# Optimization experiments

Hardware: AMD Instinct MI355X
Metric: run time of the kernel (lower is better)

## Reference

```python
import jax, jax.numpy as jnp
import numpy as np

B, N, H_IN, H_HID, N_HEAD = 32, 500, 64, 16, 8
N_VALID = 400  # valid (non-padded) nodes per graph; node 0 is the root
NEG_INF = -1e20


def setup_inputs() -> dict:
    key = jax.random.key(0)
    ks = jax.random.split(key, 10)
    x = jax.random.normal(ks[0], (B, N, H_IN), jnp.float32)
    # sparse-ish binary adjacency with self loops
    A = (jax.random.uniform(ks[1], (B, N, N)) < 0.05).astype(jnp.float32)
    A = jnp.maximum(A, jnp.eye(N, dtype=jnp.float32)[None])
    # mask_nonzero: first N_VALID nodes of every graph are valid
    mask_batch = jnp.repeat(jnp.arange(B, dtype=jnp.int32), N_VALID)
    mask_row = jnp.tile(jnp.arange(N_VALID, dtype=jnp.int32), B)
    s = 0.1
    w1 = jax.random.normal(ks[2], (N_HEAD, H_IN, H_HID), jnp.float32) * s
    a_src1 = jax.random.normal(ks[3], (N_HEAD, H_HID), jnp.float32) * s
    a_dst1 = jax.random.normal(ks[4], (N_HEAD, H_HID), jnp.float32) * s
    w2 = jax.random.normal(ks[5], (1, N_HEAD * H_HID, H_IN), jnp.float32) * s
    a_src2 = jax.random.normal(ks[6], (1, H_IN), jnp.float32) * s
    a_dst2 = jax.random.normal(ks[7], (1, H_IN), jnp.float32) * s
    attn_w = jax.random.normal(ks[8], (2 * H_IN,), jnp.float32) * s
    return {"x": x, "A": A, "mask_batch": mask_batch, "mask_row": mask_row,
            "w1": w1, "a_src1": a_src1, "a_dst1": a_dst1,
            "w2": w2, "a_src2": a_src2, "a_dst2": a_dst2, "attn_w": attn_w}


def gat_layer(h_in, A, w, a_src, a_dst):
    # h_in: [B,N,F_in]; w: [H,F_in,F_out]
    h = jnp.einsum('bnf,hfo->bhno', h_in, w)              # [B,H,N,F_out]
    e_src = jnp.einsum('bhno,ho->bhn', h, a_src)          # [B,H,N]
    e_dst = jnp.einsum('bhno,ho->bhn', h, a_dst)
    e = jax.nn.leaky_relu(e_src[..., :, None] + e_dst[..., None, :], 0.2)  # [B,H,N,N]
    e = jnp.where(A[:, None, :, :] > 0, e, NEG_INF)
    attn = jax.nn.softmax(e, axis=-1)
    return jnp.einsum('bhnm,bhmo->bhno', attn, h)         # [B,H,N,F_out]


def reference(x, A, mask_batch, mask_row, w1, a_src1, a_dst1, w2, a_src2, a_dst2, attn_w):
    b, n, _ = x.shape
    # BatchGAT encoder: layer 1 (multi-head, concat + ELU), layer 2 (1 head -> h_in)
    h1 = gat_layer(x, A, w1, a_src1, a_dst1)                       # [B,H,N,h_hid]
    h1 = jax.nn.elu(h1).transpose(0, 2, 1, 3).reshape(b, n, -1)    # [B,N,H*h_hid]
    xc = gat_layer(h1, A, w2, a_src2, a_dst2)[:, 0]                # [B,N,h_in]
    # zero out padded nodes (so their Post_Attn scores are exactly 0)
    valid = jnp.zeros((b, n), x.dtype).at[mask_batch, mask_row].set(1.0)
    xc = xc * valid[:, :, None]
    # Post_Attn: scatter root features to each valid node position
    root = jnp.zeros_like(xc).at[mask_batch, mask_row, :].set(xc[mask_batch, 0, :])
    x_plus = jnp.concatenate([xc, root], axis=-1)                  # [B,N,2*h_in]
    score = x_plus @ attn_w                                        # [B,N]
    score = jnp.where(score == 0, NEG_INF, score)[:, :, None]      # masked_fill
    attn = jax.nn.softmax(score, axis=1)                           # softmax over nodes
    pooled = jnp.einsum('bnf,bn->bf', xc, attn[:, :, 0])           # [B,h_in]
    return pooled, attn
```

## Files before the change

kernel.cpp:

```cpp
#include <hip/hip_runtime.h>

#define NB 32
#define NN 500
#define HIN 64
#define HHID 16
#define NHEAD 8
#define NVALID 400
#define MAXK 128
#define NEG_INF -1e20f

__global__ __launch_bounds__(256) void k_nbr(const float* __restrict__ A,
                                             int* __restrict__ nbr, int* __restrict__ cnt)
{
    int row = blockIdx.x * 4 + (threadIdx.x >> 6);
    int lane = threadIdx.x & 63;
    if (row >= NB * NN) return;
    const float* arow = A + (size_t)row * NN;
    int c = 0;
    for (int it = 0; it < 8; ++it) {
        int m = it * 64 + lane;
        bool v = (m < NN) && (arow[m] > 0.0f);
        unsigned long long bal = __ballot(v);
        if (v) {
            int pos = c + __popcll(bal & ((1ull << lane) - 1ull));
            if (pos < MAXK) nbr[(size_t)row * MAXK + pos] = m;
        }
        c += (int)__popcll(bal);
    }
    if (lane == 0) cnt[row] = c < MAXK ? c : MAXK;
}

__global__ __launch_bounds__(256) void k_proj1(const float* __restrict__ x, const float* __restrict__ w1,
                                               const float* __restrict__ as1, const float* __restrict__ ad1,
                                               float* __restrict__ h1p, float* __restrict__ e1s,
                                               float* __restrict__ e1d)
{
    int b = blockIdx.y, chunk = blockIdx.x;
    int t = threadIdx.x, slot = t >> 7, lane = t & 127;
    int h = lane >> 4, o = lane & 15;
    float wreg[64];
#pragma unroll
    for (int f = 0; f < 64; ++f) wreg[f] = w1[h * 1024 + f * 16 + o];
    float as_r = as1[h * 16 + o], ad_r = ad1[h * 16 + o];
    __shared__ __align__(16) float xs[2][64];
    for (int i = 0; i < 8; ++i) {
        int n = chunk * 16 + i * 2 + slot;
        bool valid = n < NN;
        if (valid && lane < 64) xs[slot][lane] = x[(size_t)(b * NN + n) * HIN + lane];
        __syncthreads();
        if (valid) {
            float acc = 0.f;
#pragma unroll
            for (int f4 = 0; f4 < 16; ++f4) {
                float4 xv = *(const float4*)&xs[slot][f4 * 4];
                acc += xv.x * wreg[f4 * 4] + xv.y * wreg[f4 * 4 + 1]
                     + xv.z * wreg[f4 * 4 + 2] + xv.w * wreg[f4 * 4 + 3];
            }
            h1p[((size_t)(b * NHEAD + h) * NN + n) * HHID + o] = acc;
            float vs = acc * as_r, vd = acc * ad_r;
#pragma unroll
            for (int m = 1; m < 16; m <<= 1) { vs += __shfl_xor(vs, m); vd += __shfl_xor(vd, m); }
            if (o == 0) {
                e1s[(size_t)(b * NHEAD + h) * NN + n] = vs;
                e1d[(size_t)(b * NHEAD + h) * NN + n] = vd;
            }
        }
        __syncthreads();
    }
}

__global__ __launch_bounds__(128) void k_agg1(const int* __restrict__ nbr, const int* __restrict__ cnt,
                                              const float* __restrict__ h1p, const float* __restrict__ e1s,
                                              const float* __restrict__ e1d, float* __restrict__ h1cat)
{
    int row = blockIdx.x;
    int b = row / NN, n = row - b * NN;
    int t = threadIdx.x;
    __shared__ int nb_s[MAXK];
    __shared__ float p_s[NHEAD][MAXK];
    __shared__ float stat[NHEAD][2];
    int K = cnt[row];
    for (int k = t; k < K; k += 128) nb_s[k] = nbr[(size_t)row * MAXK + k];
    __syncthreads();
    for (int idx = t; idx < NHEAD * K; idx += 128) {
        int h = idx / K, k = idx - h * K;
        float e = e1s[(size_t)(b * NHEAD + h) * NN + n]
                + e1d[(size_t)(b * NHEAD + h) * NN + nb_s[k]];
        p_s[h][k] = e > 0.f ? e : 0.2f * e;
    }
    __syncthreads();
    if (t < NHEAD) {
        float mx = -1e30f;
        for (int k = 0; k < K; ++k) mx = fmaxf(mx, p_s[t][k]);
        float sum = 0.f;
        for (int k = 0; k < K; ++k) sum += __expf(p_s[t][k] - mx);
        stat[t][0] = mx; stat[t][1] = 1.f / sum;
    }
    __syncthreads();
    for (int idx = t; idx < NHEAD * K; idx += 128) {
        int h = idx / K, k = idx - h * K;
        p_s[h][k] = __expf(p_s[h][k] - stat[h][0]) * stat[h][1];
    }
    __syncthreads();
    int h = t >> 4, o = t & 15;
    float acc = 0.f;
    const float* hp = h1p + (size_t)(b * NHEAD + h) * NN * HHID + o;
    for (int k = 0; k < K; ++k) acc += p_s[h][k] * hp[(size_t)nb_s[k] * HHID];
    float outv = acc > 0.f ? acc : expm1f(acc);
    h1cat[(size_t)row * (NHEAD * HHID) + t] = outv;
}

__global__ __launch_bounds__(256) void k_proj2(const float* __restrict__ h1cat, const float* __restrict__ w2,
                                               const float* __restrict__ as2, const float* __restrict__ ad2,
                                               float* __restrict__ h2p, float* __restrict__ e2s,
                                               float* __restrict__ e2d)
{
    int b = blockIdx.y, chunk = blockIdx.x;
    int t = threadIdx.x, slot = t >> 7, lane = t & 127;
    int fh = lane >> 6, o = lane & 63;
    float wreg[64];
#pragma unroll
    for (int j = 0; j < 64; ++j) wreg[j] = w2[(fh * 64 + j) * 64 + o];
    float as_r = as2[o], ad_r = ad2[o];
    __shared__ __align__(16) float xs[2][128];
    __shared__ float part[2][128];
    for (int i = 0; i < 8; ++i) {
        int n = chunk * 16 + i * 2 + slot;
        bool valid = n < NN;
        if (valid) xs[slot][lane] = h1cat[(size_t)(b * NN + n) * 128 + lane];
        __syncthreads();
        float acc = 0.f;
        if (valid) {
#pragma unroll
            for (int j4 = 0; j4 < 16; ++j4) {
                float4 xv = *(const float4*)&xs[slot][fh * 64 + j4 * 4];
                acc += xv.x * wreg[j4 * 4] + xv.y * wreg[j4 * 4 + 1]
                     + xv.z * wreg[j4 * 4 + 2] + xv.w * wreg[j4 * 4 + 3];
            }
        }
        part[slot][lane] = acc;
        __syncthreads();
        if (valid && fh == 0) {
            float val = acc + part[slot][64 + o];
            h2p[(size_t)(b * NN + n) * 64 + o] = val;
            float vs = val * as_r, vd = val * ad_r;
#pragma unroll
            for (int m = 1; m < 64; m <<= 1) { vs += __shfl_xor(vs, m); vd += __shfl_xor(vd, m); }
            if (o == 0) { e2s[b * NN + n] = vs; e2d[b * NN + n] = vd; }
        }
        __syncthreads();
    }
}

__global__ __launch_bounds__(64) void k_agg2(const int* __restrict__ nbr, const int* __restrict__ cnt,
                                             const float* __restrict__ h2p, const float* __restrict__ e2s,
                                             const float* __restrict__ e2d, const float* __restrict__ aw,
                                             float* __restrict__ xc, float* __restrict__ sc,
                                             float* __restrict__ root_dot)
{
    int row = blockIdx.x;
    int b = row / NN, n = row - b * NN;
    int t = threadIdx.x;
    if (n >= NVALID) { xc[(size_t)row * 64 + t] = 0.f; return; }
    __shared__ int nb_s[MAXK];
    __shared__ float p_s[MAXK];
    __shared__ float stat[2];
    int K = cnt[row];
    for (int k = t; k < K; k += 64) nb_s[k] = nbr[(size_t)row * MAXK + k];
    __syncthreads();
    float es = e2s[row];
    for (int k = t; k < K; k += 64) {
        float e = es + e2d[b * NN + nb_s[k]];
        p_s[k] = e > 0.f ? e : 0.2f * e;
    }
    __syncthreads();
    if (t == 0) {
        float mx = -1e30f;
        for (int k = 0; k < K; ++k) mx = fmaxf(mx, p_s[k]);
        float sum = 0.f;
        for (int k = 0; k < K; ++k) sum += __expf(p_s[k] - mx);
        stat[0] = mx; stat[1] = 1.f / sum;
    }
    __syncthreads();
    for (int k = t; k < K; k += 64) p_s[k] = __expf(p_s[k] - stat[0]) * stat[1];
    __syncthreads();
    float acc = 0.f;
    for (int k = 0; k < K; ++k) acc += p_s[k] * h2p[(size_t)(b * NN + nb_s[k]) * 64 + t];
    xc[(size_t)row * 64 + t] = acc;
    float v = acc * aw[t];
#pragma unroll
    for (int m = 1; m < 64; m <<= 1) v += __shfl_xor(v, m);
    if (t == 0) sc[row] = v;
    if (n == 0) {
        float v2 = acc * aw[64 + t];
#pragma unroll
        for (int m = 1; m < 64; m <<= 1) v2 += __shfl_xor(v2, m);
        if (t == 0) root_dot[b] = v2;
    }
}

__global__ __launch_bounds__(1024) void k_pool(const float* __restrict__ xc, const float* __restrict__ sc,
                                               const float* __restrict__ root_dot, float* __restrict__ out)
{
    int b = blockIdx.x;
    int t = threadIdx.x, w = t >> 6, lane = t & 63;
    __shared__ float attn_s[NN];
    __shared__ float red[16];
    __shared__ float part[16][64];
    const float* xb = xc + (size_t)b * NN * 64;
    float rd = root_dot[b];
    float s = NEG_INF;
    if (t < NVALID) {
        s = sc[b * NN + t] + rd;
        if (s == 0.f) s = NEG_INF;
    }
    float mx = s;
#pragma unroll
    for (int m = 1; m < 64; m <<= 1) mx = fmaxf(mx, __shfl_xor(mx, m));
    if (lane == 0) red[w] = mx;
    __syncthreads();
    mx = red[0];
#pragma unroll
    for (int i = 1; i < 16; ++i) mx = fmaxf(mx, red[i]);
    float e = (t < NN) ? __expf(s - mx) : 0.f;
    float sum = e;
#pragma unroll
    for (int m = 1; m < 64; m <<= 1) sum += __shfl_xor(sum, m);
    __syncthreads();
    if (lane == 0) red[w] = sum;
    __syncthreads();
    sum = 0.f;
#pragma unroll
    for (int i = 0; i < 16; ++i) sum += red[i];
    float inv = 1.f / sum;
    if (t < NN) {
        float a = e * inv;
        out[NB * 64 + b * NN + t] = a;
        attn_s[t] = a;
    }
    __syncthreads();
    float acc = 0.f;
    for (int n = w; n < NN; n += 16) acc += attn_s[n] * xb[(size_t)n * 64 + lane];
    part[w][lane] = acc;
    __syncthreads();
    if (t < 64) {
        float v = 0.f;
#pragma unroll
        for (int i = 0; i < 16; ++i) v += part[i][t];
        out[b * 64 + t] = v;
    }
}

extern "C" void kernel_launch(void* const* d_in, const int* in_sizes, int n_in,
                              void* d_out, int out_size, void* d_ws, size_t ws_size,
                              hipStream_t stream) {
    const float* x   = (const float*)d_in[0];
    const float* A   = (const float*)d_in[1];
    const float* w1  = (const float*)d_in[4];
    const float* as1 = (const float*)d_in[5];
    const float* ad1 = (const float*)d_in[6];
    const float* w2  = (const float*)d_in[7];
    const float* as2 = (const float*)d_in[8];
    const float* ad2 = (const float*)d_in[9];
    const float* aw  = (const float*)d_in[10];
    float* out = (float*)d_out;

    char* ws = (char*)d_ws;
    int* nbr = (int*)ws;
    int* cnt = (int*)(ws + (size_t)16000 * 128 * 4);
    float* f = (float*)(ws + (size_t)16000 * 129 * 4);
    float* h1p   = f;  f += (size_t)NB * NHEAD * NN * HHID;
    float* e1s   = f;  f += (size_t)NB * NHEAD * NN;
    float* e1d   = f;  f += (size_t)NB * NHEAD * NN;
    float* h1cat = f;  f += (size_t)NB * NN * 128;
    float* h2p   = f;  f += (size_t)NB * NN * 64;
    float* e2s   = f;  f += (size_t)NB * NN;
    float* e2d   = f;  f += (size_t)NB * NN;
    float* xc    = f;  f += (size_t)NB * NN * 64;
    float* sc    = f;  f += (size_t)NB * NN;
    float* rootd = f;  f += NB;

    hipLaunchKernelGGL(k_nbr,   dim3(4000),   dim3(256), 0, stream, A, nbr, cnt);
    hipLaunchKernelGGL(k_proj1, dim3(32, NB), dim3(256), 0, stream, x, w1, as1, ad1, h1p, e1s, e1d);
    hipLaunchKernelGGL(k_agg1,  dim3(NB * NN), dim3(128), 0, stream, nbr, cnt, h1p, e1s, e1d, h1cat);
    hipLaunchKernelGGL(k_proj2, dim3(32, NB), dim3(256), 0, stream, h1cat, w2, as2, ad2, h2p, e2s, e2d);
    hipLaunchKernelGGL(k_agg2,  dim3(NB * NN), dim3(64), 0, stream, nbr, cnt, h2p, e2s, e2d, aw, xc, sc, rootd);
    hipLaunchKernelGGL(k_pool,  dim3(NB),     dim3(1024), 0, stream, xc, sc, rootd, out);
}
```

Baseline: 186.9 us.

## Merge neighbor-list and projection kernels, node-major layout, register softmax in aggregations

Merges the adjacency scan and the layer-1 projection into one launch, with block ID deciding the role. The adjacency scan now reads rows as float4. The h1p and e1s/e1d buffers switch to node-major layout so each neighbor gather in agg1 reads 128 contiguous floats instead of strided per-head rows. The softmax in both aggregation kernels now runs in registers with warp shuffles instead of serial single-thread loops and extra barriers. This cuts launch count, serial reduction time and uncoalesced gathers, but assumes at most 128 neighbors, matching MAXK.

```diff
diff --git a/kernel.cpp b/kernel.cpp
--- a/kernel.cpp
+++ b/kernel.cpp
@@ -9,33 +9,44 @@
 #define MAXK 128
 #define NEG_INF -1e20f
 
-__global__ __launch_bounds__(256) void k_nbr(const float* __restrict__ A,
-                                             int* __restrict__ nbr, int* __restrict__ cnt)
-{
-    int row = blockIdx.x * 4 + (threadIdx.x >> 6);
-    int lane = threadIdx.x & 63;
-    if (row >= NB * NN) return;
-    const float* arow = A + (size_t)row * NN;
-    int c = 0;
-    for (int it = 0; it < 8; ++it) {
-        int m = it * 64 + lane;
-        bool v = (m < NN) && (arow[m] > 0.0f);
-        unsigned long long bal = __ballot(v);
-        if (v) {
-            int pos = c + __popcll(bal & ((1ull << lane) - 1ull));
-            if (pos < MAXK) nbr[(size_t)row * MAXK + pos] = m;
-        }
-        c += (int)__popcll(bal);
-    }
-    if (lane == 0) cnt[row] = c < MAXK ? c : MAXK;
-}
-
-__global__ __launch_bounds__(256) void k_proj1(const float* __restrict__ x, const float* __restrict__ w1,
-                                               const float* __restrict__ as1, const float* __restrict__ ad1,
-                                               float* __restrict__ h1p, float* __restrict__ e1s,
-                                               float* __restrict__ e1d)
-{
-    int b = blockIdx.y, chunk = blockIdx.x;
+__global__ __launch_bounds__(256) void k_pre(const float* __restrict__ A,
+                                             int* __restrict__ nbr, int* __restrict__ cnt,
+                                             const float* __restrict__ x, const float* __restrict__ w1,
+                                             const float* __restrict__ as1, const float* __restrict__ ad1,
+                                             float* __restrict__ h1p, float* __restrict__ e1s,
+                                             float* __restrict__ e1d)
+{
+    int bid = blockIdx.x;
+    if (bid < 4000) {
+        int row = bid * 4 + (threadIdx.x >> 6);
+        int lane = threadIdx.x & 63;
+        const float4* arow4 = (const float4*)(A + (size_t)row * NN);
+        int* np = nbr + (size_t)row * MAXK;
+        int c = 0;
+#pragma unroll
+        for (int it = 0; it < 2; ++it) {
+            int idx = it * 64 + lane;
+            float4 av;
+            if (idx < 125) av = arow4[idx];
+            else { av.x = av.y = av.z = av.w = 0.f; }
+            bool v0 = av.x > 0.f, v1 = av.y > 0.f, v2 = av.z > 0.f, v3 = av.w > 0.f;
+            unsigned long long b0 = __ballot(v0), b1 = __ballot(v1);
+            unsigned long long b2 = __ballot(v2), b3 = __ballot(v3);
+            unsigned long long below = (1ull << lane) - 1ull;
+            int p = c + __popcll(b0 & below) + __popcll(b1 & below)
+                      + __popcll(b2 & below) + __popcll(b3 & below);
+            int col = idx * 4;
+            if (v0 && p < MAXK) np[p] = col;     p += (int)v0;
+            if (v1 && p < MAXK) np[p] = col + 1; p += (int)v1;
+            if (v2 && p < MAXK) np[p] = col + 2; p += (int)v2;
+            if (v3 && p < MAXK) np[p] = col + 3; p += (int)v3;
+            c += (int)(__popcll(b0) + __popcll(b1) + __popcll(b2) + __popcll(b3));
+        }
+        if (lane == 0) cnt[row] = c < MAXK ? c : MAXK;
+        return;
+    }
+    int pb = bid - 4000;
+    int b = pb >> 5, chunk = pb & 31;
     int t = threadIdx.x, slot = t >> 7, lane = t & 127;
     int h = lane >> 4, o = lane & 15;
     float wreg[64];
@@ -56,13 +67,13 @@
                 acc += xv.x * wreg[f4 * 4] + xv.y * wreg[f4 * 4 + 1]
                      + xv.z * wreg[f4 * 4 + 2] + xv.w * wreg[f4 * 4 + 3];
             }
-            h1p[((size_t)(b * NHEAD + h) * NN + n) * HHID + o] = acc;
+            h1p[(size_t)(b * NN + n) * 128 + lane] = acc;
             float vs = acc * as_r, vd = acc * ad_r;
 #pragma unroll
             for (int m = 1; m < 16; m <<= 1) { vs += __shfl_xor(vs, m); vd += __shfl_xor(vd, m); }
             if (o == 0) {
-                e1s[(size_t)(b * NHEAD + h) * NN + n] = vs;
-                e1d[(size_t)(b * NHEAD + h) * NN + n] = vd;
+                e1s[(size_t)(b * NN + n) * 8 + h] = vs;
+                e1d[(size_t)(b * NN + n) * 8 + h] = vd;
             }
         }
         __syncthreads();
@@ -75,39 +86,49 @@
 {
     int row = blockIdx.x;
     int b = row / NN, n = row - b * NN;
+    (void)n;
     int t = threadIdx.x;
+    int h = t >> 4, o = t & 15;
     __shared__ int nb_s[MAXK];
     __shared__ float p_s[NHEAD][MAXK];
-    __shared__ float stat[NHEAD][2];
     int K = cnt[row];
     for (int k = t; k < K; k += 128) nb_s[k] = nbr[(size_t)row * MAXK + k];
     __syncthreads();
-    for (int idx = t; idx < NHEAD * K; idx += 128) {
-        int h = idx / K, k = idx - h * K;
-        float e = e1s[(size_t)(b * NHEAD + h) * NN + n]
-                + e1d[(size_t)(b * NHEAD + h) * NN + nb_s[k]];
-        p_s[h][k] = e > 0.f ? e : 0.2f * e;
-    }
-    __syncthreads();
-    if (t < NHEAD) {
-        float mx = -1e30f;
-        for (int k = 0; k < K; ++k) mx = fmaxf(mx, p_s[t][k]);
-        float sum = 0.f;
-        for (int k = 0; k < K; ++k) sum += __expf(p_s[t][k] - mx);
-        stat[t][0] = mx; stat[t][1] = 1.f / sum;
-    }
-    __syncthreads();
-    for (int idx = t; idx < NHEAD * K; idx += 128) {
-        int h = idx / K, k = idx - h * K;
-        p_s[h][k] = __expf(p_s[h][k] - stat[h][0]) * stat[h][1];
-    }
-    __syncthreads();
-    int h = t >> 4, o = t & 15;
+    float es = e1s[(size_t)row * 8 + h];
+    float r[8];
+    float mx = -1e30f;
+#pragma unroll
+    for (int j = 0; j < 8; ++j) {
+        int k = o + j * 16;
+        if (k < K) {
+            float e = es + e1d[(size_t)(b * NN + nb_s[k]) * 8 + h];
+            e = e > 0.f ? e : 0.2f * e;
+            r[j] = e;
+            mx = fmaxf(mx, e);
+        }
+    }
+#pragma unroll
+    for (int m = 1; m < 16; m <<= 1) mx = fmaxf(mx, __shfl_xor(mx, m));
+    float sum = 0.f;
+#pragma unroll
+    for (int j = 0; j < 8; ++j) {
+        int k = o + j * 16;
+        if (k < K) { float v = __expf(r[j] - mx); r[j] = v; sum += v; }
+    }
+#pragma unroll
+    for (int m = 1; m < 16; m <<= 1) sum += __shfl_xor(sum, m);
+    float inv = 1.f / sum;
+#pragma unroll
+    for (int j = 0; j < 8; ++j) {
+        int k = o + j * 16;
+        if (k < K) p_s[h][k] = r[j] * inv;
+    }
+    __syncthreads();
     float acc = 0.f;
-    const float* hp = h1p + (size_t)(b * NHEAD + h) * NN * HHID + o;
-    for (int k = 0; k < K; ++k) acc += p_s[h][k] * hp[(size_t)nb_s[k] * HHID];
+    const float* hp = h1p + (size_t)b * NN * 128 + t;
+    for (int k = 0; k < K; ++k) acc += p_s[h][k] * hp[(size_t)nb_s[k] * 128];
     float outv = acc > 0.f ? acc : expm1f(acc);
-    h1cat[(size_t)row * (NHEAD * HHID) + t] = outv;
+    h1cat[(size_t)row * 128 + t] = outv;
 }
 
 __global__ __launch_bounds__(256) void k_proj2(const float* __restrict__ h1cat, const float* __restrict__ w2,
@@ -164,25 +185,30 @@
     if (n >= NVALID) { xc[(size_t)row * 64 + t] = 0.f; return; }
     __shared__ int nb_s[MAXK];
     __shared__ float p_s[MAXK];
-    __shared__ float stat[2];
     int K = cnt[row];
     for (int k = t; k < K; k += 64) nb_s[k] = nbr[(size_t)row * MAXK + k];
     __syncthreads();
     float es = e2s[row];
-    for (int k = t; k < K; k += 64) {
-        float e = es + e2d[b * NN + nb_s[k]];
-        p_s[k] = e > 0.f ? e : 0.2f * e;
-    }
-    __syncthreads();
-    if (t == 0) {
-        float mx = -1e30f;
-        for (int k = 0; k < K; ++k) mx = fmaxf(mx, p_s[k]);
-        float sum = 0.f;
-        for (int k = 0; k < K; ++k) sum += __expf(p_s[k] - mx);
-        stat[0] = mx; stat[1] = 1.f / sum;
-    }
-    __syncthreads();
-    for (int k = t; k < K; k += 64) p_s[k] = __expf(p_s[k] - stat[0]) * stat[1];
+    float r0 = -1e30f, r1 = -1e30f;
+    if (t < K) {
+        float e = es + e2d[b * NN + nb_s[t]];
+        r0 = e > 0.f ? e : 0.2f * e;
+    }
+    if (t + 64 < K) {
+        float e = es + e2d[b * NN + nb_s[t + 64]];
+        r1 = e > 0.f ? e : 0.2f * e;
+    }
+    float mx = fmaxf(r0, r1);
+#pragma unroll
+    for (int m = 1; m < 64; m <<= 1) mx = fmaxf(mx, __shfl_xor(mx, m));
+    float v0 = (t < K) ? __expf(r0 - mx) : 0.f;
+    float v1 = (t + 64 < K) ? __expf(r1 - mx) : 0.f;
+    float sum = v0 + v1;
+#pragma unroll
+    for (int m = 1; m < 64; m <<= 1) sum += __shfl_xor(sum, m);
+    float inv = 1.f / sum;
+    if (t < K) p_s[t] = v0 * inv;
+    if (t + 64 < K) p_s[t + 64] = v1 * inv;
     __syncthreads();
     float acc = 0.f;
     for (int k = 0; k < K; ++k) acc += p_s[k] * h2p[(size_t)(b * NN + nb_s[k]) * 64 + t];
@@ -269,9 +295,9 @@
     int* nbr = (int*)ws;
     int* cnt = (int*)(ws + (size_t)16000 * 128 * 4);
     float* f = (float*)(ws + (size_t)16000 * 129 * 4);
-    float* h1p   = f;  f += (size_t)NB * NHEAD * NN * HHID;
-    float* e1s   = f;  f += (size_t)NB * NHEAD * NN;
-    float* e1d   = f;  f += (size_t)NB * NHEAD * NN;
+    float* h1p   = f;  f += (size_t)NB * NN * 128;
+    float* e1s   = f;  f += (size_t)NB * NN * NHEAD;
+    float* e1d   = f;  f += (size_t)NB * NN * NHEAD;
     float* h1cat = f;  f += (size_t)NB * NN * 128;
     float* h2p   = f;  f += (size_t)NB * NN * 64;
     float* e2s   = f;  f += (size_t)NB * NN;
@@ -280,8 +306,7 @@
     float* sc    = f;  f += (size_t)NB * NN;
     float* rootd = f;  f += NB;
 
-    hipLaunchKernelGGL(k_nbr,   dim3(4000),   dim3(256), 0, stream, A, nbr, cnt);
-    hipLaunchKernelGGL(k_proj1, dim3(32, NB), dim3(256), 0, stream, x, w1, as1, ad1, h1p, e1s, e1d);
+    hipLaunchKernelGGL(k_pre,   dim3(5024),   dim3(256), 0, stream, A, nbr, cnt, x, w1, as1, ad1, h1p, e1s, e1d);
     hipLaunchKernelGGL(k_agg1,  dim3(NB * NN), dim3(128), 0, stream, nbr, cnt, h1p, e1s, e1d, h1cat);
     hipLaunchKernelGGL(k_proj2, dim3(32, NB), dim3(256), 0, stream, h1cat, w2, as2, ad2, h2p, e2s, e2d);
     hipLaunchKernelGGL(k_agg2,  dim3(NB * NN), dim3(64), 0, stream, nbr, cnt, h2p, e2s, e2d, aw, xc, sc, rootd);
```

Result: faster. 169.5 us (-9.3%).
